# Kernel optimization log

Measured on AMD Instinct MI355X. Metric: run time of the kernel, lower is better.

Reference implementation:

```python
import jax, jax.numpy as jnp
import numpy as np


def _chamfer(src, tgt):
    # src: [B, N, 3], tgt: [B, M, 3]
    x2 = jnp.sum(src * src, axis=-1)              # [B, N]
    y2 = jnp.sum(tgt * tgt, axis=-1)              # [B, M]
    xy = jnp.einsum('bnd,bmd->bnm', src, tgt)     # [B, N, M]
    d2 = x2[:, :, None] + y2[:, None, :] - 2.0 * xy
    d2 = jnp.maximum(d2, 0.0)                     # guard tiny negatives
    cham_x = jnp.min(d2, axis=2)                  # [B, N] min over tgt
    cham_y = jnp.min(d2, axis=1)                  # [B, M] min over src
    # point_reduction='mean', batch_reduction='sum'
    loss = jnp.sum(jnp.mean(cham_x, axis=1)) + jnp.sum(jnp.mean(cham_y, axis=1))
    return loss


def setup_inputs() -> dict:
    key = jax.random.key(0)
    k1, k2 = jax.random.split(key)
    src = jax.random.normal(k1, (16, 4096, 3), dtype=jnp.float32)
    tgt = jax.random.normal(k2, (16, 4096, 3), dtype=jnp.float32)
    return {"src": src, "tgt": tgt}


def reference(src, tgt):
    wgeo = 1.0
    return wgeo * _chamfer(src, tgt)
```

## Files before the change

kernel.cpp:

```cpp
#include <hip/hip_runtime.h>
#include <hip/hip_bf16.h>


#define BATCH   16
#define NPTS    4096
#define CHUNKC  512
#define COLSPB  2048
#define NCHUNKS (COLSPB / CHUNKC)
#define NSTRIPS 16
#define NMINS   (2 * BATCH * NPTS)

typedef __attribute__((ext_vector_type(8)))  short short8;
typedef __attribute__((ext_vector_type(16))) float float16;

union U4S8 { uint4 u; short8 s; };

__device__ inline unsigned int bfb(float v) {
    __hip_bfloat16 h = __float2bfloat16(v);
    unsigned short u; __builtin_memcpy(&u, &h, 2);
    return (unsigned int)u;
}
__device__ inline float bff(float v) { return __bfloat162float(__float2bfloat16(v)); }

#define ONEB 0x3F80u

__device__ inline void buildA(float x, float y, float z, uint4& w0, uint4& w1) {
    float xhf = bff(x), yhf = bff(y), zhf = bff(z);
    float f = fmaf(x, x, fmaf(y, y, z * z));
    float fhf = bff(f);
    unsigned xh = bfb(xhf), yh = bfb(yhf), zh = bfb(zhf);
    unsigned xl = bfb(x - xhf), yl = bfb(y - yhf), zl = bfb(z - zhf);
    unsigned fh = bfb(fhf), fl = bfb(f - fhf);
    w0 = make_uint4(xh | (yh << 16), zh | (xh << 16),
                    yh | (zh << 16), xl | (yl << 16));
    w1 = make_uint4(zl | (fh << 16), fl | (ONEB << 16), ONEB, 0u);
}

__device__ inline void buildB(float x, float y, float z, uint4& w0, uint4& w1) {
    float xhf = bff(x), yhf = bff(y), zhf = bff(z);
    float f = fmaf(x, x, fmaf(y, y, z * z));
    float fhf = bff(f);
    unsigned a = bfb(-2.0f * xhf), b = bfb(-2.0f * yhf), c = bfb(-2.0f * zhf);
    unsigned d = bfb(-2.0f * (x - xhf)), e = bfb(-2.0f * (y - yhf)),
             g = bfb(-2.0f * (z - zhf));
    unsigned fh = bfb(fhf), fl = bfb(f - fhf);
    w0 = make_uint4(a | (b << 16), c | (d << 16),
                    e | (g << 16), a | (b << 16));
    w1 = make_uint4(c | (ONEB << 16), ONEB | (fh << 16), fl, 0u);
}

__global__ __launch_bounds__(256, 4) void chamfer_mfma_kernel(
    const float* __restrict__ src, const float* __restrict__ tgt,
    unsigned int* __restrict__ mins)
{
    __shared__ uint4 sbuf[2][2][CHUNKC];

    int blk = blockIdx.x;
    const int ch    = blk & 1;             blk >>= 1;
    const int strip = blk & (NSTRIPS - 1); blk >>= 4;
    const int b     = blk & 15;            blk >>= 4;
    const int dir   = blk;

    const int lane = threadIdx.x & 63;
    const int w    = threadIdx.x >> 6;
    const int half = lane >> 5;
    const int l5   = lane & 31;

    const float* Araw = (dir ? tgt : src) + (size_t)b * NPTS * 3;
    const float* Braw = (dir ? src : tgt) + (size_t)b * NPTS * 3;
    const int colbase = ch * COLSPB;

    short8 afr[2];
#pragma unroll
    for (int g = 0; g < 2; g++) {
        int row = strip * 256 + g * 128 + w * 32 + l5;
        uint4 w0, w1;
        buildA(Araw[3 * row], Araw[3 * row + 1], Araw[3 * row + 2], w0, w1);
        U4S8 t; t.u = half ? w1 : w0;
        afr[g] = t.s;
    }

    float nx[2][3];
    auto loadRaw = [&](int c) {
#pragma unroll
        for (int k = 0; k < 2; k++) {
            int p = colbase + c * CHUNKC + (int)threadIdx.x + k * 256;
            nx[k][0] = Braw[3 * p + 0];
            nx[k][1] = Braw[3 * p + 1];
            nx[k][2] = Braw[3 * p + 2];
        }
    };
    auto convertWrite = [&](int bi) {
#pragma unroll
        for (int k = 0; k < 2; k++) {
            int lp = (int)threadIdx.x + k * 256;
            uint4 w0, w1;
            buildB(nx[k][0], nx[k][1], nx[k][2], w0, w1);
            sbuf[bi][0][lp] = w0;
            sbuf[bi][1][lp] = w1;
        }
    };

    const float16 z16 = {0.f,0.f,0.f,0.f,0.f,0.f,0.f,0.f,
                         0.f,0.f,0.f,0.f,0.f,0.f,0.f,0.f};
    float rm[2][16];
#pragma unroll
    for (int g = 0; g < 2; g++)
#pragma unroll
        for (int r = 0; r < 16; r++) rm[g][r] = 1e30f;

    loadRaw(0);
    convertWrite(0);
    for (int c = 0; c < NCHUNKS; c++) {
        __syncthreads();
        if (c + 1 < NCHUNKS) loadRaw(c + 1);
        const int bi = c & 1;
#pragma unroll 2
        for (int j2 = 0; j2 < CHUNKC / 64; j2++) {
            U4S8 t0, t1;
            t0.u = sbuf[bi][half][j2 * 64 + l5];
            t1.u = sbuf[bi][half][j2 * 64 + 32 + l5];
#pragma unroll
            for (int g = 0; g < 2; g++) {
                float16 a0 = __builtin_amdgcn_mfma_f32_32x32x16_bf16(afr[g], t0.s, z16, 0, 0, 0);
                float16 a1 = __builtin_amdgcn_mfma_f32_32x32x16_bf16(afr[g], t1.s, z16, 0, 0, 0);
#pragma unroll
                for (int r = 0; r < 16; r++)
                    rm[g][r] = fminf(fminf(a0[r], a1[r]), rm[g][r]);
            }
        }
        if (c + 1 < NCHUNKS) convertWrite((c + 1) & 1);
    }

#pragma unroll
    for (int mask = 1; mask <= 16; mask <<= 1)
#pragma unroll
        for (int g = 0; g < 2; g++)
#pragma unroll
            for (int r = 0; r < 16; r++)
                rm[g][r] = fminf(rm[g][r], __shfl_xor(rm[g][r], mask, 64));

    if (l5 == 0) {
        unsigned int* mrow = mins + (size_t)(dir * BATCH + b) * NPTS;
#pragma unroll
        for (int g = 0; g < 2; g++)
#pragma unroll
            for (int r = 0; r < 16; r++) {
                int row = strip * 256 + g * 128 + w * 32 + (r & 3) + 8 * (r >> 2) + 4 * half;
                float v = fmaxf(rm[g][r], 0.0f);
                atomicMin(&mrow[row], __float_as_uint(v));
            }
    }
}

__global__ __launch_bounds__(256) void chamfer_reduce_kernel(
    const unsigned int* __restrict__ mins, float* __restrict__ out)
{
    float s = 0.0f;
    for (int idx = blockIdx.x * blockDim.x + threadIdx.x; idx < NMINS;
         idx += gridDim.x * blockDim.x) {
        s += __uint_as_float(mins[idx]);
    }
#pragma unroll
    for (int off = 32; off > 0; off >>= 1) s += __shfl_down(s, off, 64);
    __shared__ float wsum[4];
    int lane = threadIdx.x & 63;
    int w = threadIdx.x >> 6;
    if (lane == 0) wsum[w] = s;
    __syncthreads();
    if (threadIdx.x == 0) {
        float tot = wsum[0] + wsum[1] + wsum[2] + wsum[3];
        atomicAdd(out, tot * (1.0f / (float)NPTS));
    }
}

extern "C" void kernel_launch(void* const* d_in, const int* in_sizes, int n_in,
                              void* d_out, int out_size, void* d_ws, size_t ws_size,
                              hipStream_t stream)
{
    const float* src = (const float*)d_in[0];
    const float* tgt = (const float*)d_in[1];
    float* out = (float*)d_out;
    unsigned int* mins = (unsigned int*)d_ws;

    hipMemsetAsync(mins, 0xFF, (size_t)NMINS * sizeof(unsigned int), stream);
    hipMemsetAsync(out, 0, sizeof(float), stream);

    chamfer_mfma_kernel<<<2 * BATCH * NSTRIPS * 2, 256, 0, stream>>>(src, tgt, mins);
    chamfer_reduce_kernel<<<128, 256, 0, stream>>>(mins, out);
}
```

Before: 83.84 us.

## Fuse final reduction into chamfer kernel with last-block ticket counters

Removes the separate reduction kernel and the second memset. Each pair of column-half blocks writes its row minima to a per-strip buffer, and the second block to finish a pair, found through an atomic ticket, sums that strip. A global ticket then picks the last strip block to sum all strip partials and write the output. The raw B loads are also issued earlier, before building A fragments and before the barrier, to overlap global latency. This trades a kernel launch and a full-array pass for extra atomics, fences and a serialized tail in one block.

```diff
diff --git a/kernel.cpp b/kernel.cpp
--- a/kernel.cpp
+++ b/kernel.cpp
@@ -8,7 +8,7 @@
 #define COLSPB  2048
 #define NCHUNKS (COLSPB / CHUNKC)
 #define NSTRIPS 16
-#define NMINS   (2 * BATCH * NPTS)
+#define NPAIRS  (2 * BATCH * NSTRIPS)
 
 typedef __attribute__((ext_vector_type(8)))  short short8;
 typedef __attribute__((ext_vector_type(16))) float float16;
@@ -49,20 +49,28 @@
     w1 = make_uint4(c | (ONEB << 16), ONEB | (fh << 16), fl, 0u);
 }
 
-__global__ __launch_bounds__(256, 4) void chamfer_mfma_kernel(
+__global__ __launch_bounds__(256, 4) void chamfer_kernel(
     const float* __restrict__ src, const float* __restrict__ tgt,
-    unsigned int* __restrict__ mins)
+    unsigned int* __restrict__ pairmin,
+    unsigned int* __restrict__ ptick,
+    unsigned int* __restrict__ gtick,
+    unsigned int* __restrict__ pairsum,
+    float* __restrict__ out)
 {
     __shared__ uint4 sbuf[2][2][CHUNKC];
+    __shared__ float wsum[4];
+    __shared__ int flag;
 
     int blk = blockIdx.x;
     const int ch    = blk & 1;             blk >>= 1;
     const int strip = blk & (NSTRIPS - 1); blk >>= 4;
     const int b     = blk & 15;            blk >>= 4;
     const int dir   = blk;
-
-    const int lane = threadIdx.x & 63;
-    const int w    = threadIdx.x >> 6;
+    const int pair  = ((dir * BATCH + b) * NSTRIPS) + strip;
+
+    const int t    = threadIdx.x;
+    const int lane = t & 63;
+    const int w    = t >> 6;
     const int half = lane >> 5;
     const int l5   = lane & 31;
 
@@ -70,21 +78,11 @@
     const float* Braw = (dir ? src : tgt) + (size_t)b * NPTS * 3;
     const int colbase = ch * COLSPB;
 
-    short8 afr[2];
-#pragma unroll
-    for (int g = 0; g < 2; g++) {
-        int row = strip * 256 + g * 128 + w * 32 + l5;
-        uint4 w0, w1;
-        buildA(Araw[3 * row], Araw[3 * row + 1], Araw[3 * row + 2], w0, w1);
-        U4S8 t; t.u = half ? w1 : w0;
-        afr[g] = t.s;
-    }
-
     float nx[2][3];
     auto loadRaw = [&](int c) {
 #pragma unroll
         for (int k = 0; k < 2; k++) {
-            int p = colbase + c * CHUNKC + (int)threadIdx.x + k * 256;
+            int p = colbase + c * CHUNKC + t + k * 256;
             nx[k][0] = Braw[3 * p + 0];
             nx[k][1] = Braw[3 * p + 1];
             nx[k][2] = Braw[3 * p + 2];
@@ -93,7 +91,7 @@
     auto convertWrite = [&](int bi) {
 #pragma unroll
         for (int k = 0; k < 2; k++) {
-            int lp = (int)threadIdx.x + k * 256;
+            int lp = t + k * 256;
             uint4 w0, w1;
             buildB(nx[k][0], nx[k][1], nx[k][2], w0, w1);
             sbuf[bi][0][lp] = w0;
@@ -101,6 +99,18 @@
         }
     };
 
+    loadRaw(0);
+
+    short8 afr[2];
+#pragma unroll
+    for (int g = 0; g < 2; g++) {
+        int row = strip * 256 + g * 128 + w * 32 + l5;
+        uint4 w0, w1;
+        buildA(Araw[3 * row], Araw[3 * row + 1], Araw[3 * row + 2], w0, w1);
+        U4S8 tt; tt.u = half ? w1 : w0;
+        afr[g] = tt.s;
+    }
+
     const float16 z16 = {0.f,0.f,0.f,0.f,0.f,0.f,0.f,0.f,
                          0.f,0.f,0.f,0.f,0.f,0.f,0.f,0.f};
     float rm[2][16];
@@ -109,11 +119,10 @@
 #pragma unroll
         for (int r = 0; r < 16; r++) rm[g][r] = 1e30f;
 
-    loadRaw(0);
     convertWrite(0);
     for (int c = 0; c < NCHUNKS; c++) {
+        if (c + 1 < NCHUNKS) loadRaw(c + 1);
         __syncthreads();
-        if (c + 1 < NCHUNKS) loadRaw(c + 1);
         const int bi = c & 1;
 #pragma unroll 2
         for (int j2 = 0; j2 < CHUNKC / 64; j2++) {
@@ -141,37 +150,52 @@
                 rm[g][r] = fminf(rm[g][r], __shfl_xor(rm[g][r], mask, 64));
 
     if (l5 == 0) {
-        unsigned int* mrow = mins + (size_t)(dir * BATCH + b) * NPTS;
+        unsigned int* pm = pairmin + (size_t)pair * 256;
 #pragma unroll
         for (int g = 0; g < 2; g++)
 #pragma unroll
             for (int r = 0; r < 16; r++) {
-                int row = strip * 256 + g * 128 + w * 32 + (r & 3) + 8 * (r >> 2) + 4 * half;
+                int idx = g * 128 + w * 32 + (r & 3) + 8 * (r >> 2) + 4 * half;
                 float v = fmaxf(rm[g][r], 0.0f);
-                atomicMin(&mrow[row], __float_as_uint(v));
+                atomicMin(&pm[idx], __float_as_uint(v));
             }
     }
-}
-
-__global__ __launch_bounds__(256) void chamfer_reduce_kernel(
-    const unsigned int* __restrict__ mins, float* __restrict__ out)
-{
-    float s = 0.0f;
-    for (int idx = blockIdx.x * blockDim.x + threadIdx.x; idx < NMINS;
-         idx += gridDim.x * blockDim.x) {
-        s += __uint_as_float(mins[idx]);
-    }
-#pragma unroll
-    for (int off = 32; off > 0; off >>= 1) s += __shfl_down(s, off, 64);
-    __shared__ float wsum[4];
-    int lane = threadIdx.x & 63;
-    int w = threadIdx.x >> 6;
-    if (lane == 0) wsum[w] = s;
-    __syncthreads();
-    if (threadIdx.x == 0) {
-        float tot = wsum[0] + wsum[1] + wsum[2] + wsum[3];
-        atomicAdd(out, tot * (1.0f / (float)NPTS));
-    }
+
+    __threadfence();
+    if (t == 0) {
+        unsigned int old = atomicAdd(&ptick[pair], 1u);
+        flag = (old == 0u);
+    }
+    __syncthreads();
+    if (!flag) return;
+
+    {
+        float s = __uint_as_float(atomicMin(&pairmin[(size_t)pair * 256 + t], 0xFFFFFFFFu));
+#pragma unroll
+        for (int off = 32; off > 0; off >>= 1) s += __shfl_down(s, off, 64);
+        if ((t & 63) == 0) wsum[t >> 6] = s;
+    }
+    __syncthreads();
+    if (t == 0) {
+        float ps = wsum[0] + wsum[1] + wsum[2] + wsum[3];
+        atomicExch(&pairsum[pair], __float_as_uint(ps));
+        __threadfence();
+        unsigned int old = atomicAdd(gtick, 1u);
+        flag = (old == (unsigned int)(NPAIRS - 2));
+    }
+    __syncthreads();
+    if (!flag) return;
+
+    {
+        float s = __uint_as_float(atomicMin(&pairsum[t], 0xFFFFFFFFu))
+                + __uint_as_float(atomicMin(&pairsum[t + 256], 0xFFFFFFFFu));
+#pragma unroll
+        for (int off = 32; off > 0; off >>= 1) s += __shfl_down(s, off, 64);
+        if ((t & 63) == 0) wsum[t >> 6] = s;
+    }
+    __syncthreads();
+    if (t == 0)
+        out[0] = (wsum[0] + wsum[1] + wsum[2] + wsum[3]) * (1.0f / (float)NPTS);
 }
 
 extern "C" void kernel_launch(void* const* d_in, const int* in_sizes, int n_in,
@@ -181,11 +205,16 @@
     const float* src = (const float*)d_in[0];
     const float* tgt = (const float*)d_in[1];
     float* out = (float*)d_out;
-    unsigned int* mins = (unsigned int*)d_ws;
-
-    hipMemsetAsync(mins, 0xFF, (size_t)NMINS * sizeof(unsigned int), stream);
-    hipMemsetAsync(out, 0, sizeof(float), stream);
-
-    chamfer_mfma_kernel<<<2 * BATCH * NSTRIPS * 2, 256, 0, stream>>>(src, tgt, mins);
-    chamfer_reduce_kernel<<<128, 256, 0, stream>>>(mins, out);
-}
+
+    unsigned int* pairmin = (unsigned int*)d_ws;
+    unsigned int* ptick   = pairmin + NPAIRS * 256;
+    unsigned int* gtick   = ptick + NPAIRS;
+    unsigned int* pairsum = gtick + 1;
+
+    hipMemsetAsync(pairmin, 0xFF,
+                   (size_t)(NPAIRS * 256 + NPAIRS + 1 + NPAIRS) * sizeof(unsigned int),
+                   stream);
+
+    chamfer_kernel<<<2 * BATCH * NSTRIPS * 2, 256, 0, stream>>>(
+        src, tgt, pairmin, ptick, gtick, pairsum, out);
+}
```

After: 142.6 us. 1.7x slower.
